# Optimization experiments

Hardware: AMD Instinct MI355X
Metric: run time of the kernel (lower is better)

## Reference

```python
import jax, jax.numpy as jnp
import numpy as np

NUM_GRAPHS = 128
NUM_LAYERS = 3
D_IN = 64
D_H = 64
D_OUT = 10
N_NODES = 100000
N_EDGES = 1000000


def segment_softmax(scores, seg, num_segments):
    # numerically stable softmax over variable-size segments (per-destination-node)
    m = jax.ops.segment_max(scores, seg, num_segments=num_segments)
    ex = jnp.exp(scores - m[seg])
    s = jax.ops.segment_sum(ex, seg, num_segments=num_segments)
    return ex / (s[seg] + 1e-16)


def setup_inputs() -> dict:
    key = jax.random.key(0)
    ks = jax.random.split(key, 16)
    x = jax.random.normal(ks[0], (N_NODES, D_IN), dtype=jnp.float32)
    edge_index = jax.random.randint(ks[1], (2, N_EDGES), 0, N_NODES, dtype=jnp.int32)
    batch = jnp.sort(jax.random.randint(ks[2], (N_NODES,), 0, NUM_GRAPHS, dtype=jnp.int32))
    s = 0.05
    # stacked per-layer TransformerConv params (input_dim == hidden_dim so shapes align)
    Wq = jax.random.normal(ks[3], (NUM_LAYERS, D_H, D_H), dtype=jnp.float32) * s
    bq = jnp.zeros((NUM_LAYERS, D_H), dtype=jnp.float32)
    Wk = jax.random.normal(ks[4], (NUM_LAYERS, D_H, D_H), dtype=jnp.float32) * s
    bk = jnp.zeros((NUM_LAYERS, D_H), dtype=jnp.float32)
    Wv = jax.random.normal(ks[5], (NUM_LAYERS, D_H, D_H), dtype=jnp.float32) * s
    bv = jnp.zeros((NUM_LAYERS, D_H), dtype=jnp.float32)
    Ws = jax.random.normal(ks[6], (NUM_LAYERS, D_H, D_H), dtype=jnp.float32) * s  # root/skip lin
    bs = jnp.zeros((NUM_LAYERS, D_H), dtype=jnp.float32)
    W1 = jax.random.normal(ks[7], (D_H, D_H), dtype=jnp.float32) * s
    b1 = jnp.zeros((D_H,), dtype=jnp.float32)
    W2 = jax.random.normal(ks[8], (D_H, D_OUT), dtype=jnp.float32) * s
    b2 = jnp.zeros((D_OUT,), dtype=jnp.float32)
    return {"x": x, "edge_index": edge_index, "batch": batch,
            "Wq": Wq, "bq": bq, "Wk": Wk, "bk": bk, "Wv": Wv, "bv": bv,
            "Ws": Ws, "bs": bs, "W1": W1, "b1": b1, "W2": W2, "b2": b2}


def reference(x, edge_index, batch, Wq, bq, Wk, bk, Wv, bv, Ws, bs, W1, b1, W2, b2):
    n = x.shape[0]
    src, dst = edge_index[0], edge_index[1]  # PyG: edge_index[0]=source j, [1]=target i
    scale = 1.0 / jnp.sqrt(jnp.asarray(D_H, x.dtype))
    h = x
    pooled = []
    for l in range(NUM_LAYERS):
        q = h @ Wq[l] + bq[l]          # [N, d] query of target node
        k = h @ Wk[l] + bk[l]          # [N, d] key of source node
        v = h @ Wv[l] + bv[l]          # [N, d] value of source node
        scores = jnp.sum(q[dst] * k[src], axis=-1) * scale          # [E]
        alpha = segment_softmax(scores, dst, n)                     # softmax over in-edges
        agg = jax.ops.segment_sum(v[src] * alpha[:, None], dst, num_segments=n)  # [N, d]
        h = jax.nn.relu(agg + h @ Ws[l] + bs[l])                    # root_weight skip + relu
        pooled.append(jax.ops.segment_sum(h, batch, num_segments=NUM_GRAPHS))   # global_add_pool
    pooled_st = jnp.stack(pooled)                                   # [L, G, d]
    p = jax.nn.relu(pooled_st[-1] @ W1 + b1)                        # dropout p=0 / eval
    out = p @ W2 + b2                                               # [G, D_OUT]
    return out, pooled_st
```

## Files before the change

kernel.cpp:

```cpp
#include <hip/hip_runtime.h>
#include <hip/hip_bf16.h>
#include <math.h>

#define NN 100000
#define NE 1000000
#define DD 64
#define NG 128
#define NL 3

#define NBUK 196
#define EPB 2048
#define NBLK ((NE + EPB - 1) / EPB)
#define BCAP 6144
#define NDC 64
#define POOL_ROWS 128

typedef unsigned short ushort_t;
typedef unsigned int u32;
typedef __attribute__((ext_vector_type(8))) short short8v;
typedef __attribute__((ext_vector_type(2))) float f32x2;
typedef __attribute__((ext_vector_type(4))) float f32x4;
typedef __attribute__((ext_vector_type(4))) unsigned int u32x4;

__device__ __forceinline__ ushort_t f2bf(float f) {
    __hip_bfloat16 h = __float2bfloat16(f);
    return *reinterpret_cast<ushort_t*>(&h);
}
__device__ __forceinline__ unsigned cvtpk(float lo, float hi) {
    unsigned r;
    asm("v_cvt_pk_bf16_f32 %0, %1, %2" : "=v"(r) : "v"(lo), "v"(hi));
    return r;
}
__device__ __forceinline__ f32x2 bfpair(u32 u) {
    f32x2 r;
    r.x = __builtin_bit_cast(float, u << 16);
    r.y = __builtin_bit_cast(float, u & 0xffff0000u);
    return r;
}
template <bool HI>
__device__ __forceinline__ f32x2 f8pair(u32 u) {
    return __builtin_amdgcn_cvt_pk_f32_fp8(u, HI);
}
__device__ __forceinline__ float sum8(float x) {
    int v = __builtin_bit_cast(int, x);
    x += __builtin_bit_cast(float, __builtin_amdgcn_update_dpp(0, v, 0xB1, 0xF, 0xF, true));
    v = __builtin_bit_cast(int, x);
    x += __builtin_bit_cast(float, __builtin_amdgcn_update_dpp(0, v, 0x4E, 0xF, 0xF, true));
    v = __builtin_bit_cast(int, x);
    x += __builtin_bit_cast(float, __builtin_amdgcn_update_dpp(0, v, 0x141, 0xF, 0xF, true));
    return x;
}


__global__ __launch_bounds__(256) void zero_k(int* __restrict__ gcur, int* __restrict__ gdh) {
    if (blockIdx.x == 0 && threadIdx.x < NBUK) gcur[threadIdx.x] = 0;
    if (blockIdx.x == 1 && threadIdx.x < NDC) gdh[threadIdx.x] = 0;
}


__global__ __launch_bounds__(256) void fused_k(const float* __restrict__ x, ushort_t* __restrict__ hbf,
                                               const float* __restrict__ Wq, const float* __restrict__ Wk,
                                               const float* __restrict__ Wv, const float* __restrict__ Ws_,
                                               ushort_t* __restrict__ wpack,
                                               const int* __restrict__ src, const int* __restrict__ dst,
                                               u32* __restrict__ binbuf, int* __restrict__ gcur,
                                               float* __restrict__ out, int totOut,
                                               int cvtBlocks) {
    __shared__ int hist[NBUK];
    __shared__ int excl[NBUK];
    __shared__ int cur[NBUK];
    __shared__ int gbase[NBUK];
    __shared__ int tmp[256];
    __shared__ u32 pairs[EPB];
    __shared__ unsigned char bukid[EPB];

    int b = blockIdx.x, t = threadIdx.x;
    if (b < cvtBlocks) {
        int base = (b * 256 + t) * 4;
        float4 v = *(const float4*)&x[base];
        uint2 pk;
        pk.x = cvtpk(v.x, v.y);
        pk.y = cvtpk(v.z, v.w);
        *(uint2*)&hbf[base] = pk;
        return;
    }
    b -= cvtBlocks;
    if (b < NL * 4) {
        if (t < 64) {
            int mat = b & 3, layer = b >> 2;
            const float* W = ((mat == 0) ? Wq : (mat == 1) ? Wk : (mat == 2) ? Wv : Ws_) + layer * DD * DD;
#pragma unroll
            for (int ct = 0; ct < 4; ct++)
#pragma unroll
                for (int ks = 0; ks < 2; ks++)
#pragma unroll
                    for (int j = 0; j < 8; j++) {
                        float v = W[(ks * 32 + (t >> 4) * 8 + j) * DD + ct * 16 + (t & 15)];
                        wpack[((size_t)(b * 8 + ct * 2 + ks)) * 512 + t * 8 + j] = f2bf(v);
                    }
        }
        return;
    }
    b -= NL * 4;
    if (b >= NBLK) {
        int i = (b - NBLK) * 256 + t;
        if (i < totOut) out[i] = 0.f;
        return;
    }
    int e0 = b * EPB;
    int totvalid = NE - e0; if (totvalid > EPB) totvalid = EPB;

    for (int i = t; i < NBUK; i += 256) hist[i] = 0;
    __syncthreads();

    int mysrc[8], mydst[8];
#pragma unroll
    for (int i = 0; i < 8; i++) {
        int e = e0 + i * 256 + t;
        bool v = e < NE;
        mysrc[i] = v ? src[e] : -1;
        mydst[i] = v ? dst[e] : -1;
        if (v) atomicAdd(&hist[mydst[i] >> 9], 1);
    }
    __syncthreads();

    int v = (t < NBUK) ? hist[t] : 0;
    tmp[t] = v;
    __syncthreads();
#pragma unroll
    for (int off = 1; off < 256; off <<= 1) {
        int a = (t >= off) ? tmp[t - off] : 0;
        __syncthreads();
        tmp[t] += a;
        __syncthreads();
    }
    if (t < NBUK) { excl[t] = tmp[t] - v; cur[t] = tmp[t] - v; }
    __syncthreads();

#pragma unroll
    for (int i = 0; i < 8; i++) {
        if (mydst[i] >= 0) {
            int bb = mydst[i] >> 9;
            int p = atomicAdd(&cur[bb], 1);
            pairs[p] = ((u32)(mydst[i] & 511) << 17) | (u32)mysrc[i];
            bukid[p] = (unsigned char)bb;
        }
    }
    if (t < NBUK && v > 0) gbase[t] = atomicAdd(&gcur[t], v);
    __syncthreads();

    for (int i = t; i < totvalid; i += 256) {
        int bb = bukid[i];
        int idx = gbase[bb] + (i - excl[bb]);
        if (idx < BCAP) binbuf[(size_t)bb * BCAP + idx] = pairs[i];
    }
}


__global__ __launch_bounds__(256) void csr_k(const u32* __restrict__ binbuf,
                                             const int* __restrict__ gcur,
                                             int* __restrict__ rowstart,
                                             int* __restrict__ csr_src,
                                             int* __restrict__ gdh) {
    __shared__ u32 pairs[BCAP];
    __shared__ int csrb[BCAP];
    __shared__ int deg[512];
    __shared__ int excl[512];
    __shared__ int cur[512];
    __shared__ int tmp[512];
    __shared__ int bt[256];
    __shared__ int ch[NDC];
    int b = blockIdx.x;
    int t = threadIdx.x;

    int bv = 0;
    if (t < NBUK) { bv = gcur[t]; if (bv > BCAP) bv = BCAP; }
    bt[t] = bv;
    __syncthreads();
#pragma unroll
    for (int off = 1; off < 256; off <<= 1) {
        int a = (t >= off) ? bt[t - off] : 0;
        __syncthreads();
        bt[t] += a;
        __syncthreads();
    }
    int base = (b == 0) ? 0 : bt[b - 1];
    int T = bt[b] - base;
    if (b == 0 && t == 0) rowstart[NN] = bt[NBUK - 1];
    int nbase = b << 9;

    for (int i = t; i < 512; i += 256) deg[i] = 0;
    if (t < NDC) ch[t] = 0;
    for (int i = t; i < T; i += 256) pairs[i] = binbuf[(size_t)b * BCAP + i];
    __syncthreads();
    for (int i = t; i < T; i += 256) atomicAdd(&deg[pairs[i] >> 17], 1);
    __syncthreads();

    for (int i = t; i < 512; i += 256) {
        if (nbase + i < NN) {
            int d = deg[i]; if (d > NDC - 1) d = NDC - 1;
            atomicAdd(&ch[d], 1);
        }
    }

    int v0 = deg[t], v1 = deg[t + 256];
    tmp[t] = v0; tmp[t + 256] = v1;
    __syncthreads();
#pragma unroll
    for (int off = 1; off < 512; off <<= 1) {
        int a0 = (t >= off) ? tmp[t - off] : 0;
        int i1 = t + 256;
        int a1 = (i1 >= off) ? tmp[i1 - off] : 0;
        __syncthreads();
        tmp[t] += a0; tmp[i1] += a1;
        __syncthreads();
    }
    excl[t] = tmp[t] - v0; excl[t + 256] = tmp[t + 256] - v1;
    cur[t] = excl[t]; cur[t + 256] = excl[t + 256];
    if (t < NDC && ch[t]) atomicAdd(&gdh[t], ch[t]);
    __syncthreads();

    for (int i = t; i < 512; i += 256) {
        int n = nbase + i;
        if (n < NN) rowstart[n] = base + excl[i];
    }

    for (int i = t; i < T; i += 256) {
        u32 p = pairs[i];
        int pos = atomicAdd(&cur[p >> 17], 1);
        csrb[pos] = (int)(p & 0x1FFFFu);
    }
    __syncthreads();
    for (int i = t; i < T; i += 256) csr_src[base + i] = csrb[i];
}


__global__ __launch_bounds__(64) void dscan_k(const int* __restrict__ gdh,
                                              int* __restrict__ gdcur) {
    int t = threadIdx.x;
    int v = gdh[t];
    int inc = v;
#pragma unroll
    for (int off = 1; off < NDC; off <<= 1) {
        int u = __shfl_up(inc, off);
        if (t >= off) inc += u;
    }
    gdcur[t] = inc - v;
}

__global__ __launch_bounds__(256) void dperm_k(const int* __restrict__ rowstart,
                                               int* __restrict__ gdcur,
                                               int* __restrict__ perm) {
    __shared__ int h[NDC];
    __shared__ int cur[NDC];
    int t = threadIdx.x;
    if (t < NDC) h[t] = 0;
    __syncthreads();
    int n0 = blockIdx.x * 1024;
    int myd[4];
#pragma unroll
    for (int i = 0; i < 4; i++) {
        int n = n0 + i * 256 + t;
        myd[i] = -1;
        if (n < NN) {
            int d = rowstart[n + 1] - rowstart[n];
            if (d > NDC - 1) d = NDC - 1;
            myd[i] = d;
            atomicAdd(&h[d], 1);
        }
    }
    __syncthreads();
    if (t < NDC) cur[t] = h[t] ? atomicAdd(&gdcur[t], h[t]) : 0;
    __syncthreads();
#pragma unroll
    for (int i = 0; i < 4; i++) {
        if (myd[i] >= 0) {
            int pos = atomicAdd(&cur[myd[i]], 1);
            perm[pos] = n0 + i * 256 + t;
        }
    }
}


__device__ __forceinline__ void pool_body(const ushort_t* __restrict__ h,
                                          const int* __restrict__ batch,
                                          float* __restrict__ pooled, int pb) {
    int i0 = pb * POOL_ROWS;
    int i1 = i0 + POOL_ROWS; if (i1 > NN) i1 = NN;
    int lane = threadIdx.x & 63;
    int wv = threadIdx.x >> 6;
    float acc = 0.f;
    int gc = -1;
    for (int i = i0 + wv; i < i1; i += 4) {
        int gi = batch[i];
        if (gi != gc) {
            if (gc >= 0) atomicAdd(&pooled[gc * DD + lane], acc);
            gc = gi; acc = 0.f;
        }
        unsigned u = ((unsigned)h[(size_t)i * DD + lane]) << 16;
        acc += __builtin_bit_cast(float, u);
    }
    if (gc >= 0) atomicAdd(&pooled[gc * DD + lane], acc);
}


__global__ __launch_bounds__(256) void gemm4pool_k(const ushort_t* __restrict__ hbf,
                                                   const ushort_t* __restrict__ wpl,
                                                   const float* __restrict__ bq_, const float* __restrict__ bk_,
                                                   const float* __restrict__ bv_, const float* __restrict__ bs_,
                                                   ushort_t* __restrict__ qo, unsigned char* __restrict__ kv8,
                                                   ushort_t* __restrict__ so,
                                                   const int* __restrict__ batch,
                                                   float* __restrict__ pooledPrev, int gtiles) {
    __shared__ char stage[4][2304];
    int blk = blockIdx.x;
    if (blk >= gtiles) {
        pool_body(hbf, batch, pooledPrev, blk - gtiles);
        return;
    }
    int t = threadIdx.x;
    int lane = t & 63, wv = t >> 6;
    int ln = lane & 15, lq = lane >> 4;
    int rowbase = blk * 64;
    char* st = stage[wv];
    bool isbf = (wv == 0) || (wv == 3);
    int kvoff = (wv == 1) ? 0 : 64;

    const float* bsel = (wv == 0) ? bq_ : (wv == 1) ? bk_ : (wv == 2) ? bv_ : bs_;
    ushort_t* osel    = (wv == 0) ? qo : so;

    short8v wfrag[4][2];
#pragma unroll
    for (int ct = 0; ct < 4; ct++)
#pragma unroll
        for (int ks = 0; ks < 2; ks++)
            wfrag[ct][ks] = *(const short8v*)&wpl[((size_t)(wv * 8 + ct * 2 + ks)) * 512 + lane * 8];

    float4 bias[4];
#pragma unroll
    for (int ct = 0; ct < 4; ct++) bias[ct] = *(const float4*)&bsel[ct * 16 + lq * 4];

#pragma unroll
    for (int rt = 0; rt < 4; rt++) {
        int grow0 = rowbase + rt * 16 + ln;
        int gr = grow0 < NN ? grow0 : NN - 1;
        short8v h0 = *(const short8v*)&hbf[(size_t)gr * DD + lq * 8];
        short8v h1 = *(const short8v*)&hbf[(size_t)gr * DD + 32 + lq * 8];
#pragma unroll
        for (int ct = 0; ct < 4; ct++) {
            f32x4 acc;
            acc[0] = bias[ct].x; acc[1] = bias[ct].y; acc[2] = bias[ct].z; acc[3] = bias[ct].w;
            acc = __builtin_amdgcn_mfma_f32_16x16x32_bf16(wfrag[ct][0], h0, acc, 0, 0, 0);
            acc = __builtin_amdgcn_mfma_f32_16x16x32_bf16(wfrag[ct][1], h1, acc, 0, 0, 0);
            if (isbf) {
                uint2 pk;
                pk.x = cvtpk(acc[0], acc[1]);
                pk.y = cvtpk(acc[2], acc[3]);
                *(uint2*)(st + ln * 144 + ct * 32 + lq * 8) = pk;
            } else {
                int pk8 = __builtin_amdgcn_cvt_pk_fp8_f32(acc[0], acc[1], 0, false);
                pk8 = __builtin_amdgcn_cvt_pk_fp8_f32(acc[2], acc[3], pk8, true);
                *(u32*)(st + ln * 80 + ct * 16 + lq * 4) = (u32)pk8;
            }
        }
        if (isbf) {
#pragma unroll
            for (int hh = 0; hh < 2; hh++) {
                int r = (lane >> 3) + 8 * hh;
                int c = lane & 7;
                u32x4 d = *(const u32x4*)(st + r * 144 + c * 16);
                int grow = rowbase + rt * 16 + r;
                if (grow < NN) *(u32x4*)&osel[(size_t)grow * DD + c * 8] = d;
            }
        } else {
            int r = lane >> 2;
            int c = lane & 3;
            u32x4 d = *(const u32x4*)(st + r * 80 + c * 16);
            int grow = rowbase + rt * 16 + r;
            if (grow < NN) *(u32x4*)(kv8 + (size_t)grow * 128 + kvoff + c * 16) = d;
        }
    }
}


#define SCLOG2E 0.18033688011112042f

__global__ __launch_bounds__(256) void agg_k(const ushort_t* __restrict__ qb,
                                             const unsigned char* __restrict__ kv8,
                                             const ushort_t* __restrict__ skb,
                                             const int* __restrict__ rowstart,
                                             const int* __restrict__ csr_src,
                                             const int* __restrict__ perm,
                                             ushort_t* __restrict__ hout) {
    int wv = threadIdx.x >> 6, lane = threadIdx.x & 63;
    int g = lane >> 3, j = lane & 7, sub = g & 1;
    int slot = blockIdx.x * 16 + wv * 4 + (g >> 1);
    if (slot >= NN) return;
    int nid = perm[(NN - 1) - slot];
    int r0 = rowstart[nid];
    int r1 = rowstart[nid + 1];

    u32x4 qa = *(const u32x4*)(qb + ((u32)nid << 6) + ((u32)j << 3));
    f32x2 q0 = bfpair(qa.x), q1 = bfpair(qa.y), q2 = bfpair(qa.z), q3 = bfpair(qa.w);

    float m = -1.0e38f, se = 0.f;
    f32x2 a0 = {0.f, 0.f}, a1 = {0.f, 0.f}, a2 = {0.f, 0.f}, a3 = {0.f, 0.f};

    int clampE = r1 - 1; if (clampE < 0) clampE = 0;
    int e = r0 + sub * 2;
    int sA0 = csr_src[e     < clampE ? e     : clampE];
    int sA1 = csr_src[e + 1 < clampE ? e + 1 : clampE];
    int sB0 = csr_src[e + 4 < clampE ? e + 4 : clampE];
    int sB1 = csr_src[e + 5 < clampE ? e + 5 : clampE];
    int sC0 = csr_src[e + 8 < clampE ? e + 8 : clampE];
    int sC1 = csr_src[e + 9 < clampE ? e + 9 : clampE];
    int sD0 = csr_src[e + 12 < clampE ? e + 12 : clampE];
    int sD1 = csr_src[e + 13 < clampE ? e + 13 : clampE];
    uint2 kA0 = *(const uint2*)(kv8 + (size_t)sA0 * 128 + 8 * j);
    uint2 vA0 = *(const uint2*)(kv8 + (size_t)sA0 * 128 + 64 + 8 * j);
    uint2 kA1 = *(const uint2*)(kv8 + (size_t)sA1 * 128 + 8 * j);
    uint2 vA1 = *(const uint2*)(kv8 + (size_t)sA1 * 128 + 64 + 8 * j);
    uint2 kB0 = *(const uint2*)(kv8 + (size_t)sB0 * 128 + 8 * j);
    uint2 vB0 = *(const uint2*)(kv8 + (size_t)sB0 * 128 + 64 + 8 * j);
    uint2 kB1 = *(const uint2*)(kv8 + (size_t)sB1 * 128 + 8 * j);
    uint2 vB1 = *(const uint2*)(kv8 + (size_t)sB1 * 128 + 64 + 8 * j);

    while (__ballot(e < r1)) {
        int e16 = e + 16;
        int sE0 = csr_src[e16     < clampE ? e16     : clampE];
        int sE1 = csr_src[e16 + 1 < clampE ? e16 + 1 : clampE];
        uint2 kC0 = *(const uint2*)(kv8 + (size_t)sC0 * 128 + 8 * j);
        uint2 vC0 = *(const uint2*)(kv8 + (size_t)sC0 * 128 + 64 + 8 * j);
        uint2 kC1 = *(const uint2*)(kv8 + (size_t)sC1 * 128 + 8 * j);
        uint2 vC1 = *(const uint2*)(kv8 + (size_t)sC1 * 128 + 64 + 8 * j);

        f32x2 d0 = q0 * f8pair<false>(kA0.x);
        d0 += q1 * f8pair<true >(kA0.x);
        d0 += q2 * f8pair<false>(kA0.y);
        d0 += q3 * f8pair<true >(kA0.y);
        f32x2 d1 = q0 * f8pair<false>(kA1.x);
        d1 += q1 * f8pair<true >(kA1.x);
        d1 += q2 * f8pair<false>(kA1.y);
        d1 += q3 * f8pair<true >(kA1.y);
        float dp0 = sum8(d0.x + d0.y);
        float dp1 = sum8(d1.x + d1.y);

        bool act0 = e < r1, act1 = e + 1 < r1;
        float sc0 = dp0 * SCLOG2E, sc1 = dp1 * SCLOG2E;
        float s0a = act0 ? sc0 : -1.0e38f;
        float s1a = act1 ? sc1 : -1.0e38f;
        float pm = fmaxf(s0a, s1a);
        float w0 = 0.f, w1 = 0.f;
        if (pm > -1.0e37f) {
            if (pm <= m + 11.5f) {
                if (act0) w0 = exp2f(sc0 - m);
                if (act1) w1 = exp2f(sc1 - m);
            } else {
                float cc = exp2f(m - pm);
                se *= cc; a0 *= cc; a1 *= cc; a2 *= cc; a3 *= cc;
                m = pm;
                if (act0) w0 = exp2f(sc0 - pm);
                if (act1) w1 = exp2f(sc1 - pm);
            }
        }
        se += w0 + w1;
        a0 += f8pair<false>(vA0.x) * w0 + f8pair<false>(vA1.x) * w1;
        a1 += f8pair<true >(vA0.x) * w0 + f8pair<true >(vA1.x) * w1;
        a2 += f8pair<false>(vA0.y) * w0 + f8pair<false>(vA1.y) * w1;
        a3 += f8pair<true >(vA0.y) * w0 + f8pair<true >(vA1.y) * w1;

        e += 4;
        sC0 = sD0; sC1 = sD1; sD0 = sE0; sD1 = sE1;
        kA0 = kB0; vA0 = vB0; kA1 = kB1; vA1 = vB1;
        kB0 = kC0; vB0 = vC0; kB1 = kC1; vB1 = vC1;
    }

    float M = fmaxf(m, __shfl_xor(m, 8));
    float cc = exp2f(m - M);
    se *= cc; a0 *= cc; a1 *= cc; a2 *= cc; a3 *= cc;
    se += __shfl_xor(se, 8);
    a0.x += __shfl_xor(a0.x, 8); a0.y += __shfl_xor(a0.y, 8);
    a1.x += __shfl_xor(a1.x, 8); a1.y += __shfl_xor(a1.y, 8);
    a2.x += __shfl_xor(a2.x, 8); a2.y += __shfl_xor(a2.y, 8);
    a3.x += __shfl_xor(a3.x, 8); a3.y += __shfl_xor(a3.y, 8);

    if (sub == 0) {
        float inv = 1.0f / (se + 1e-16f);
        u32x4 sk = *(const u32x4*)(skb + ((u32)nid << 6) + ((u32)j << 3));
        f32x2 o0 = a0 * inv + bfpair(sk.x);
        f32x2 o1 = a1 * inv + bfpair(sk.y);
        f32x2 o2 = a2 * inv + bfpair(sk.z);
        f32x2 o3 = a3 * inv + bfpair(sk.w);
        u32x4 pk;
        pk.x = cvtpk(fmaxf(o0.x, 0.f), fmaxf(o0.y, 0.f));
        pk.y = cvtpk(fmaxf(o1.x, 0.f), fmaxf(o1.y, 0.f));
        pk.z = cvtpk(fmaxf(o2.x, 0.f), fmaxf(o2.y, 0.f));
        pk.w = cvtpk(fmaxf(o3.x, 0.f), fmaxf(o3.y, 0.f));
        *(u32x4*)(hout + ((u32)nid << 6) + ((u32)j << 3)) = pk;
    }
}


__global__ __launch_bounds__(256) void pool_k(const ushort_t* __restrict__ h,
                                              const int* __restrict__ batch,
                                              float* __restrict__ pooled) {
    pool_body(h, batch, pooled, blockIdx.x);
}


__global__ __launch_bounds__(64) void head_k(const float* __restrict__ pooled2,
                                             const float* __restrict__ W1,
                                             const float* __restrict__ b1,
                                             const float* __restrict__ W2,
                                             const float* __restrict__ b2,
                                             float* __restrict__ out) {
    int g = blockIdx.x;
    int c = threadIdx.x;
    __shared__ float pg[64], p[64];
    pg[c] = pooled2[g * DD + c];
    __syncthreads();
    float a = b1[c];
#pragma unroll 8
    for (int kk = 0; kk < 64; kk++) a += pg[kk] * W1[kk * DD + c];
    p[c] = fmaxf(a, 0.f);
    __syncthreads();
    if (c < 10) {
        float o = b2[c];
#pragma unroll 8
        for (int kk = 0; kk < 64; kk++) o += p[kk] * W2[kk * 10 + c];
        out[g * 10 + c] = o;
    }
}


extern "C" void kernel_launch(void* const* d_in, const int* in_sizes, int n_in,
                              void* d_out, int out_size, void* d_ws, size_t ws_size,
                              hipStream_t stream) {
    const float* x    = (const float*)d_in[0];
    const int*   ei   = (const int*)d_in[1];
    const int*   batch= (const int*)d_in[2];
    const float* Wq   = (const float*)d_in[3];
    const float* bq   = (const float*)d_in[4];
    const float* Wk   = (const float*)d_in[5];
    const float* bk   = (const float*)d_in[6];
    const float* Wv   = (const float*)d_in[7];
    const float* bv   = (const float*)d_in[8];
    const float* Wsp  = (const float*)d_in[9];
    const float* bsp  = (const float*)d_in[10];
    const float* W1   = (const float*)d_in[11];
    const float* b1   = (const float*)d_in[12];
    const float* W2   = (const float*)d_in[13];
    const float* b2   = (const float*)d_in[14];
    float* out = (float*)d_out;
    float* pooled = out + NG * 10;

    const int* srcv = ei;
    const int* dstv = ei + NE;

    const size_t NEL = (size_t)NN * DD;
    ushort_t* hbf = (ushort_t*)d_ws;
    ushort_t* qb  = hbf + NEL;
    ushort_t* skb = qb  + NEL;
    unsigned char* kv8 = (unsigned char*)(skb + NEL);
    u32* binbuf   = (u32*)(kv8 + (size_t)NN * 128);
    int* gcur     = (int*)(binbuf + (size_t)NBUK * BCAP);
    int* gdh      = gcur + NBUK;
    int* gdcur    = gdh + NDC;
    int* rowstart = gdcur + NDC;
    int* csr_src  = rowstart + (NN + 1);
    int* perm     = csr_src + NE;
    ushort_t* wpack = (ushort_t*)(perm + NN);

    int totOut = NG * 10 + NL * NG * DD;
    int cvtBlocks = (int)(NEL / 4 / 256);
    int zeroBlocks = (totOut + 255) / 256;

    zero_k<<<2, 256, 0, stream>>>(gcur, gdh);
    fused_k<<<cvtBlocks + NL * 4 + NBLK + zeroBlocks, 256, 0, stream>>>(
        x, hbf, Wq, Wk, Wv, Wsp, wpack, srcv, dstv, binbuf, gcur, out, totOut, cvtBlocks);
    csr_k<<<NBUK, 256, 0, stream>>>(binbuf, gcur, rowstart, csr_src, gdh);
    dscan_k<<<1, 64, 0, stream>>>(gdh, gdcur);
    dperm_k<<<(NN + 1023) / 1024, 256, 0, stream>>>(rowstart, gdcur, perm);

    int gtiles = (NN + 63) / 64;
    int poolblocks = (NN + POOL_ROWS - 1) / POOL_ROWS;
    for (int l = 0; l < NL; l++) {
        int extra = (l > 0) ? poolblocks : 0;
        gemm4pool_k<<<gtiles + extra, 256, 0, stream>>>(
            hbf, wpack + (size_t)l * 4 * 8 * 512,
            bq + l * DD, bk + l * DD, bv + l * DD, bsp + l * DD,
            qb, kv8, skb, batch,
            (l > 0) ? (pooled + (l - 1) * NG * DD) : nullptr, gtiles);
        agg_k<<<(NN + 15) / 16, 256, 0, stream>>>(qb, kv8, skb, rowstart, csr_src, perm, hbf);
    }
    pool_k<<<poolblocks, 256, 0, stream>>>(hbf, batch, pooled + 2 * NG * DD);
    head_k<<<NG, 64, 0, stream>>>(pooled + 2 * NG * DD, W1, b1, W2, b2, out);
}
```

Baseline: 214.8 us.

## Fuse x bf16 conversion and degree-permutation into first GEMM; one node per 8-lane group

Drops the separate fp32-to-bf16 pass over x: the first layer's GEMM now reads fp32 x and converts in registers. The degree scan and permutation kernels are folded into extra tail blocks of the first gemm4pool launch, with each block recomputing the 64-entry prefix scan locally, which removes two launches. The aggregation kernel now assigns one destination node to each 8-lane group instead of two groups splitting the edges, which removes the cross-group softmax merge but makes each group walk its edge list serially.

```diff
diff --git a/kernel.cpp b/kernel.cpp
--- a/kernel.cpp
+++ b/kernel.cpp
@@ -14,6 +14,7 @@
 #define BCAP 6144
 #define NDC 64
 #define POOL_ROWS 128
+#define DPERM_BLOCKS ((NN + 1023) / 1024)
 
 typedef unsigned short ushort_t;
 typedef unsigned int u32;
@@ -52,20 +53,19 @@
 }
 
 
-__global__ __launch_bounds__(256) void zero_k(int* __restrict__ gcur, int* __restrict__ gdh) {
+__global__ __launch_bounds__(256) void zero_k(int* __restrict__ gcur, int* __restrict__ gdh,
+                                              int* __restrict__ gdcur) {
     if (blockIdx.x == 0 && threadIdx.x < NBUK) gcur[threadIdx.x] = 0;
-    if (blockIdx.x == 1 && threadIdx.x < NDC) gdh[threadIdx.x] = 0;
-}
-
-
-__global__ __launch_bounds__(256) void fused_k(const float* __restrict__ x, ushort_t* __restrict__ hbf,
-                                               const float* __restrict__ Wq, const float* __restrict__ Wk,
+    if (blockIdx.x == 1 && threadIdx.x < NDC) { gdh[threadIdx.x] = 0; gdcur[threadIdx.x] = 0; }
+}
+
+
+__global__ __launch_bounds__(256) void fused_k(const float* __restrict__ Wq, const float* __restrict__ Wk,
                                                const float* __restrict__ Wv, const float* __restrict__ Ws_,
                                                ushort_t* __restrict__ wpack,
                                                const int* __restrict__ src, const int* __restrict__ dst,
                                                u32* __restrict__ binbuf, int* __restrict__ gcur,
-                                               float* __restrict__ out, int totOut,
-                                               int cvtBlocks) {
+                                               float* __restrict__ out, int totOut) {
     __shared__ int hist[NBUK];
     __shared__ int excl[NBUK];
     __shared__ int cur[NBUK];
@@ -75,16 +75,6 @@
     __shared__ unsigned char bukid[EPB];
 
     int b = blockIdx.x, t = threadIdx.x;
-    if (b < cvtBlocks) {
-        int base = (b * 256 + t) * 4;
-        float4 v = *(const float4*)&x[base];
-        uint2 pk;
-        pk.x = cvtpk(v.x, v.y);
-        pk.y = cvtpk(v.z, v.w);
-        *(uint2*)&hbf[base] = pk;
-        return;
-    }
-    b -= cvtBlocks;
     if (b < NL * 4) {
         if (t < 64) {
             int mat = b & 3, layer = b >> 2;
@@ -235,28 +225,27 @@
 }
 
 
-__global__ __launch_bounds__(64) void dscan_k(const int* __restrict__ gdh,
-                                              int* __restrict__ gdcur) {
-    int t = threadIdx.x;
-    int v = gdh[t];
-    int inc = v;
-#pragma unroll
-    for (int off = 1; off < NDC; off <<= 1) {
-        int u = __shfl_up(inc, off);
-        if (t >= off) inc += u;
-    }
-    gdcur[t] = inc - v;
-}
-
-__global__ __launch_bounds__(256) void dperm_k(const int* __restrict__ rowstart,
-                                               int* __restrict__ gdcur,
-                                               int* __restrict__ perm) {
+__device__ __forceinline__ void dperm_body(const int* __restrict__ rowstart,
+                                           const int* __restrict__ gdh,
+                                           int* __restrict__ gdcur,
+                                           int* __restrict__ perm, int pb) {
     __shared__ int h[NDC];
     __shared__ int cur[NDC];
+    __shared__ int cbase[NDC];
     int t = threadIdx.x;
-    if (t < NDC) h[t] = 0;
-    __syncthreads();
-    int n0 = blockIdx.x * 1024;
+    if (t < NDC) {
+        h[t] = 0;
+        int v = gdh[t];
+        int inc = v;
+#pragma unroll
+        for (int off = 1; off < NDC; off <<= 1) {
+            int u = __shfl_up(inc, off);
+            if (t >= off) inc += u;
+        }
+        cbase[t] = inc - v;
+    }
+    __syncthreads();
+    int n0 = pb * 1024;
     int myd[4];
 #pragma unroll
     for (int i = 0; i < 4; i++) {
@@ -270,7 +259,7 @@
         }
     }
     __syncthreads();
-    if (t < NDC) cur[t] = h[t] ? atomicAdd(&gdcur[t], h[t]) : 0;
+    if (t < NDC) cur[t] = h[t] ? (cbase[t] + atomicAdd(&gdcur[t], h[t])) : 0;
     __syncthreads();
 #pragma unroll
     for (int i = 0; i < 4; i++) {
@@ -305,17 +294,23 @@
 
 
 __global__ __launch_bounds__(256) void gemm4pool_k(const ushort_t* __restrict__ hbf,
+                                                   const float* __restrict__ xf32,
                                                    const ushort_t* __restrict__ wpl,
                                                    const float* __restrict__ bq_, const float* __restrict__ bk_,
                                                    const float* __restrict__ bv_, const float* __restrict__ bs_,
                                                    ushort_t* __restrict__ qo, unsigned char* __restrict__ kv8,
                                                    ushort_t* __restrict__ so,
                                                    const int* __restrict__ batch,
-                                                   float* __restrict__ pooledPrev, int gtiles) {
+                                                   float* __restrict__ pooledPrev, int gtiles, int tailMode,
+                                                   const int* __restrict__ rowstart,
+                                                   const int* __restrict__ gdh,
+                                                   int* __restrict__ gdcur,
+                                                   int* __restrict__ perm) {
     __shared__ char stage[4][2304];
     int blk = blockIdx.x;
     if (blk >= gtiles) {
-        pool_body(hbf, batch, pooledPrev, blk - gtiles);
+        if (tailMode == 1) pool_body(hbf, batch, pooledPrev, blk - gtiles);
+        else dperm_body(rowstart, gdh, gdcur, perm, blk - gtiles);
         return;
     }
     int t = threadIdx.x;
@@ -344,8 +339,23 @@
     for (int rt = 0; rt < 4; rt++) {
         int grow0 = rowbase + rt * 16 + ln;
         int gr = grow0 < NN ? grow0 : NN - 1;
-        short8v h0 = *(const short8v*)&hbf[(size_t)gr * DD + lq * 8];
-        short8v h1 = *(const short8v*)&hbf[(size_t)gr * DD + 32 + lq * 8];
+        short8v h0, h1;
+        if (xf32) {
+            float4 f0 = *(const float4*)&xf32[(size_t)gr * DD + lq * 8];
+            float4 f1 = *(const float4*)&xf32[(size_t)gr * DD + lq * 8 + 4];
+            float4 f2 = *(const float4*)&xf32[(size_t)gr * DD + 32 + lq * 8];
+            float4 f3 = *(const float4*)&xf32[(size_t)gr * DD + 32 + lq * 8 + 4];
+            u32x4 p0, p1;
+            p0[0] = cvtpk(f0.x, f0.y); p0[1] = cvtpk(f0.z, f0.w);
+            p0[2] = cvtpk(f1.x, f1.y); p0[3] = cvtpk(f1.z, f1.w);
+            p1[0] = cvtpk(f2.x, f2.y); p1[1] = cvtpk(f2.z, f2.w);
+            p1[2] = cvtpk(f3.x, f3.y); p1[3] = cvtpk(f3.z, f3.w);
+            h0 = __builtin_bit_cast(short8v, p0);
+            h1 = __builtin_bit_cast(short8v, p1);
+        } else {
+            h0 = *(const short8v*)&hbf[(size_t)gr * DD + lq * 8];
+            h1 = *(const short8v*)&hbf[(size_t)gr * DD + 32 + lq * 8];
+        }
 #pragma unroll
         for (int ct = 0; ct < 4; ct++) {
             f32x4 acc;
@@ -393,8 +403,8 @@
                                              const int* __restrict__ perm,
                                              ushort_t* __restrict__ hout) {
     int wv = threadIdx.x >> 6, lane = threadIdx.x & 63;
-    int g = lane >> 3, j = lane & 7, sub = g & 1;
-    int slot = blockIdx.x * 16 + wv * 4 + (g >> 1);
+    int g = lane >> 3, j = lane & 7;
+    int slot = blockIdx.x * 32 + wv * 8 + g;
     if (slot >= NN) return;
     int nid = perm[(NN - 1) - slot];
     int r0 = rowstart[nid];
@@ -407,15 +417,15 @@
     f32x2 a0 = {0.f, 0.f}, a1 = {0.f, 0.f}, a2 = {0.f, 0.f}, a3 = {0.f, 0.f};
 
     int clampE = r1 - 1; if (clampE < 0) clampE = 0;
-    int e = r0 + sub * 2;
+    int e = r0;
     int sA0 = csr_src[e     < clampE ? e     : clampE];
     int sA1 = csr_src[e + 1 < clampE ? e + 1 : clampE];
-    int sB0 = csr_src[e + 4 < clampE ? e + 4 : clampE];
-    int sB1 = csr_src[e + 5 < clampE ? e + 5 : clampE];
-    int sC0 = csr_src[e + 8 < clampE ? e + 8 : clampE];
-    int sC1 = csr_src[e + 9 < clampE ? e + 9 : clampE];
-    int sD0 = csr_src[e + 12 < clampE ? e + 12 : clampE];
-    int sD1 = csr_src[e + 13 < clampE ? e + 13 : clampE];
+    int sB0 = csr_src[e + 2 < clampE ? e + 2 : clampE];
+    int sB1 = csr_src[e + 3 < clampE ? e + 3 : clampE];
+    int sC0 = csr_src[e + 4 < clampE ? e + 4 : clampE];
+    int sC1 = csr_src[e + 5 < clampE ? e + 5 : clampE];
+    int sD0 = csr_src[e + 6 < clampE ? e + 6 : clampE];
+    int sD1 = csr_src[e + 7 < clampE ? e + 7 : clampE];
     uint2 kA0 = *(const uint2*)(kv8 + (size_t)sA0 * 128 + 8 * j);
     uint2 vA0 = *(const uint2*)(kv8 + (size_t)sA0 * 128 + 64 + 8 * j);
     uint2 kA1 = *(const uint2*)(kv8 + (size_t)sA1 * 128 + 8 * j);
@@ -426,9 +436,9 @@
     uint2 vB1 = *(const uint2*)(kv8 + (size_t)sB1 * 128 + 64 + 8 * j);
 
     while (__ballot(e < r1)) {
-        int e16 = e + 16;
-        int sE0 = csr_src[e16     < clampE ? e16     : clampE];
-        int sE1 = csr_src[e16 + 1 < clampE ? e16 + 1 : clampE];
+        int e8 = e + 8;
+        int sE0 = csr_src[e8     < clampE ? e8     : clampE];
+        int sE1 = csr_src[e8 + 1 < clampE ? e8 + 1 : clampE];
         uint2 kC0 = *(const uint2*)(kv8 + (size_t)sC0 * 128 + 8 * j);
         uint2 vC0 = *(const uint2*)(kv8 + (size_t)sC0 * 128 + 64 + 8 * j);
         uint2 kC1 = *(const uint2*)(kv8 + (size_t)sC1 * 128 + 8 * j);
@@ -469,35 +479,24 @@
         a2 += f8pair<false>(vA0.y) * w0 + f8pair<false>(vA1.y) * w1;
         a3 += f8pair<true >(vA0.y) * w0 + f8pair<true >(vA1.y) * w1;
 
-        e += 4;
+        e += 2;
         sC0 = sD0; sC1 = sD1; sD0 = sE0; sD1 = sE1;
         kA0 = kB0; vA0 = vB0; kA1 = kB1; vA1 = vB1;
         kB0 = kC0; vB0 = vC0; kB1 = kC1; vB1 = vC1;
     }
 
-    float M = fmaxf(m, __shfl_xor(m, 8));
-    float cc = exp2f(m - M);
-    se *= cc; a0 *= cc; a1 *= cc; a2 *= cc; a3 *= cc;
-    se += __shfl_xor(se, 8);
-    a0.x += __shfl_xor(a0.x, 8); a0.y += __shfl_xor(a0.y, 8);
-    a1.x += __shfl_xor(a1.x, 8); a1.y += __shfl_xor(a1.y, 8);
-    a2.x += __shfl_xor(a2.x, 8); a2.y += __shfl_xor(a2.y, 8);
-    a3.x += __shfl_xor(a3.x, 8); a3.y += __shfl_xor(a3.y, 8);
-
-    if (sub == 0) {
-        float inv = 1.0f / (se + 1e-16f);
-        u32x4 sk = *(const u32x4*)(skb + ((u32)nid << 6) + ((u32)j << 3));
-        f32x2 o0 = a0 * inv + bfpair(sk.x);
-        f32x2 o1 = a1 * inv + bfpair(sk.y);
-        f32x2 o2 = a2 * inv + bfpair(sk.z);
-        f32x2 o3 = a3 * inv + bfpair(sk.w);
-        u32x4 pk;
-        pk.x = cvtpk(fmaxf(o0.x, 0.f), fmaxf(o0.y, 0.f));
-        pk.y = cvtpk(fmaxf(o1.x, 0.f), fmaxf(o1.y, 0.f));
-        pk.z = cvtpk(fmaxf(o2.x, 0.f), fmaxf(o2.y, 0.f));
-        pk.w = cvtpk(fmaxf(o3.x, 0.f), fmaxf(o3.y, 0.f));
-        *(u32x4*)(hout + ((u32)nid << 6) + ((u32)j << 3)) = pk;
-    }
+    float inv = 1.0f / (se + 1e-16f);
+    u32x4 sk = *(const u32x4*)(skb + ((u32)nid << 6) + ((u32)j << 3));
+    f32x2 o0 = a0 * inv + bfpair(sk.x);
+    f32x2 o1 = a1 * inv + bfpair(sk.y);
+    f32x2 o2 = a2 * inv + bfpair(sk.z);
+    f32x2 o3 = a3 * inv + bfpair(sk.w);
+    u32x4 pk;
+    pk.x = cvtpk(fmaxf(o0.x, 0.f), fmaxf(o0.y, 0.f));
+    pk.y = cvtpk(fmaxf(o1.x, 0.f), fmaxf(o1.y, 0.f));
+    pk.z = cvtpk(fmaxf(o2.x, 0.f), fmaxf(o2.y, 0.f));
+    pk.w = cvtpk(fmaxf(o3.x, 0.f), fmaxf(o3.y, 0.f));
+    *(u32x4*)(hout + ((u32)nid << 6) + ((u32)j << 3)) = pk;
 }
 
 
@@ -572,26 +571,25 @@
     ushort_t* wpack = (ushort_t*)(perm + NN);
 
     int totOut = NG * 10 + NL * NG * DD;
-    int cvtBlocks = (int)(NEL / 4 / 256);
     int zeroBlocks = (totOut + 255) / 256;
 
-    zero_k<<<2, 256, 0, stream>>>(gcur, gdh);
-    fused_k<<<cvtBlocks + NL * 4 + NBLK + zeroBlocks, 256, 0, stream>>>(
-        x, hbf, Wq, Wk, Wv, Wsp, wpack, srcv, dstv, binbuf, gcur, out, totOut, cvtBlocks);
+    zero_k<<<2, 256, 0, stream>>>(gcur, gdh, gdcur);
+    fused_k<<<NL * 4 + NBLK + zeroBlocks, 256, 0, stream>>>(
+        Wq, Wk, Wv, Wsp, wpack, srcv, dstv, binbuf, gcur, out, totOut);
     csr_k<<<NBUK, 256, 0, stream>>>(binbuf, gcur, rowstart, csr_src, gdh);
-    dscan_k<<<1, 64, 0, stream>>>(gdh, gdcur);
-    dperm_k<<<(NN + 1023) / 1024, 256, 0, stream>>>(rowstart, gdcur, perm);
 
     int gtiles = (NN + 63) / 64;
     int poolblocks = (NN + POOL_ROWS - 1) / POOL_ROWS;
     for (int l = 0; l < NL; l++) {
-        int extra = (l > 0) ? poolblocks : 0;
+        int tailMode = (l == 0) ? 2 : 1;
+        int extra = (l == 0) ? DPERM_BLOCKS : poolblocks;
         gemm4pool_k<<<gtiles + extra, 256, 0, stream>>>(
-            hbf, wpack + (size_t)l * 4 * 8 * 512,
+            hbf, (l == 0) ? x : nullptr, wpack + (size_t)l * 4 * 8 * 512,
             bq + l * DD, bk + l * DD, bv + l * DD, bsp + l * DD,
             qb, kv8, skb, batch,
-            (l > 0) ? (pooled + (l - 1) * NG * DD) : nullptr, gtiles);
-        agg_k<<<(NN + 15) / 16, 256, 0, stream>>>(qb, kv8, skb, rowstart, csr_src, perm, hbf);
+            (l > 0) ? (pooled + (l - 1) * NG * DD) : nullptr, gtiles, tailMode,
+            rowstart, gdh, gdcur, perm);
+        agg_k<<<(NN + 31) / 32, 256, 0, stream>>>(qb, kv8, skb, rowstart, csr_src, perm, hbf);
     }
     pool_k<<<poolblocks, 256, 0, stream>>>(hbf, batch, pooled + 2 * NG * DD);
     head_k<<<NG, 64, 0, stream>>>(pooled + 2 * NG * DD, W1, b1, W2, b2, out);
```

After: 205.7 us, median of 2. 1.04x faster.
